# Kernel optimization log

Hardware: AMD Instinct MI355X
Metric: run time of the kernel (lower is better)

## Reference

```python
import jax, jax.numpy as jnp
import numpy as np

K_NEIGHBORS = 9
BN_EPS = 1e-5


def _bn(x, g, b, m, v):
    # inference-mode BatchNorm over channel (last) axis
    return (x - m) * (g / jnp.sqrt(v + BN_EPS)) + b


def _sincos_1d(dim, pos):
    half = dim // 2
    omega = 1.0 / (10000.0 ** (jnp.arange(half, dtype=jnp.float32) / half))
    ang = pos[:, None] * omega[None, :]
    return jnp.concatenate([jnp.sin(ang), jnp.cos(ang)], axis=1)


def _pos_embed_2d(dim, H, W):
    # standard 2D sin-cos positional embedding, (N, dim)
    yy, xx = jnp.meshgrid(jnp.arange(H, dtype=jnp.float32), jnp.arange(W, dtype=jnp.float32), indexing='ij')
    emb_h = _sincos_1d(dim // 2, yy.reshape(-1))
    emb_w = _sincos_1d(dim // 2, xx.reshape(-1))
    return jnp.concatenate([emb_h, emb_w], axis=1)


def setup_inputs() -> dict:
    key = jax.random.key(0)
    ks = jax.random.split(key, 8)
    B, C, H, W = 8, 192, 56, 56
    C2 = 2 * C
    Cg = C2 // 4  # per-group channels for grouped 1x1 conv
    x = jax.random.normal(ks[0], (B, C, H, W), jnp.float32)
    inp = {
        'x': x,
        'fc1_w': jax.random.normal(ks[1], (C, C), jnp.float32) * 0.05,
        'fc1_b': jnp.zeros((C,), jnp.float32),
        'bn1_g': jnp.ones((C,), jnp.float32),
        'bn1_b': jnp.zeros((C,), jnp.float32),
        'bn1_m': jax.random.normal(ks[2], (C,), jnp.float32) * 0.1,
        'bn1_v': jax.random.uniform(ks[3], (C,), jnp.float32, 0.5, 1.5),
        'gc_w': jax.random.normal(ks[4], (4, Cg, Cg), jnp.float32) * 0.05,  # groups=4, (g, out_pg, in_pg)
        'gc_b': jnp.zeros((C2,), jnp.float32),
        'bng_g': jnp.ones((C2,), jnp.float32),
        'bng_b': jnp.zeros((C2,), jnp.float32),
        'bng_m': jax.random.normal(ks[5], (C2,), jnp.float32) * 0.1,
        'bng_v': jax.random.uniform(ks[6], (C2,), jnp.float32, 0.5, 1.5),
        'fc2_w': jax.random.normal(ks[7], (C, C2), jnp.float32) * 0.05,
        'fc2_b': jnp.zeros((C,), jnp.float32),
        'bn2_g': jnp.ones((C,), jnp.float32),
        'bn2_b': jnp.zeros((C,), jnp.float32),
        'bn2_m': jnp.zeros((C,), jnp.float32),
        'bn2_v': jnp.ones((C,), jnp.float32),
    }
    return inp


def reference(x, fc1_w, fc1_b, bn1_g, bn1_b, bn1_m, bn1_v,
              gc_w, gc_b, bng_g, bng_b, bng_m, bng_v,
              fc2_w, fc2_b, bn2_g, bn2_b, bn2_m, bn2_v):
    B, C, H, W = x.shape
    N = H * W
    shortcut = x
    # fc1: 1x1 conv + BN, working in (B, N, C) layout
    h = x.reshape(B, C, N).transpose(0, 2, 1)
    h = jnp.einsum('bnc,dc->bnd', h, fc1_w) + fc1_b
    h = _bn(h, bn1_g, bn1_b, bn1_m, bn1_v)
    # relative position bias (ViG-style: -2*pe@pe.T/dim)
    pe = _pos_embed_2d(C, H, W)                      # (N, C)
    rel = (-2.0 / C) * (pe @ pe.T)                   # (N, N)
    # dense dilated kNN graph on L2-normalized features
    xn = h / jnp.maximum(jnp.linalg.norm(h, axis=-1, keepdims=True), 1e-12)
    sq = jnp.sum(xn * xn, axis=-1, keepdims=True)    # (B, N, 1)
    dist = sq - 2.0 * jnp.einsum('bnc,bmc->bnm', xn, xn) + sq.transpose(0, 2, 1)
    dist = dist + rel[None]                          # (B, N, N)
    _, nn_idx = jax.lax.top_k(-dist, K_NEIGHBORS)    # (B, N, K), dilation=1
    # MRConv2d: max-relative aggregation
    x_j = h[jnp.arange(B)[:, None, None], nn_idx]    # (B, N, K, C) gather
    d = jnp.max(x_j - h[:, :, None, :], axis=2)      # (B, N, C)
    g = jnp.concatenate([h, d], axis=-1)             # (B, N, 2C)
    # grouped 1x1 conv (groups=4) + BN + GELU
    C2 = 2 * C
    Cg = C2 // 4
    gg = g.reshape(B, N, 4, Cg)
    y = jnp.einsum('bngc,gdc->bngd', gg, gc_w).reshape(B, N, C2) + gc_b
    y = jax.nn.gelu(_bn(y, bng_g, bng_b, bng_m, bng_v), approximate=False)
    # fc2: 1x1 conv + BN, residual
    o = jnp.einsum('bnc,dc->bnd', y, fc2_w) + fc2_b
    o = _bn(o, bn2_g, bn2_b, bn2_m, bn2_v)
    out = o.transpose(0, 2, 1).reshape(B, C, H, W) + shortcut
    return out
```

## Files before the change

### kernel.cpp

```cpp
#include <hip/hip_runtime.h>
#include <math.h>

#define BATCH 8
#define CH    192
#define WW    56
#define NPTS  3136
#define C2    384
#define CG    96
#define MT    32
#define MSPLIT 4
#define LK    12
#define NCAND (MSPLIT*LK)
#define NREF  16
#define MQ    (NPTS/MSPLIT)

typedef float f32x4 __attribute__((ext_vector_type(4)));
typedef short bf16x8 __attribute__((ext_vector_type(8)));

__device__ __forceinline__ float gelu_exact(float v) {
  return 0.5f * v * (1.0f + erff(v * 0.7071067811865475f));
}
__device__ __forceinline__ unsigned short f2bf(float f) {
  unsigned int u = __float_as_uint(f);
  u = u + 0x7fffu + ((u >> 16) & 1u);
  return (unsigned short)(u >> 16);
}
__device__ __forceinline__ float bf2f(unsigned short h) {
  return __uint_as_float(((unsigned int)h) << 16);
}
__device__ __forceinline__ void gl_lds16(const void* g, void* lds) {
  __builtin_amdgcn_global_load_lds(
      (const __attribute__((address_space(1))) unsigned int*)g,
      (__attribute__((address_space(3))) unsigned int*)lds, 16, 0, 0);
}
__device__ __forceinline__ unsigned fmono(float f) {
  unsigned u = __float_as_uint(f);
  return u ^ ((unsigned)((int)u >> 31) | 0x80000000u);
}
__device__ __forceinline__ unsigned umin32(unsigned a, unsigned b) { return a < b ? a : b; }
__device__ __forceinline__ unsigned umax32(unsigned a, unsigned b) { return a < b ? b : a; }

__global__ void prep_kernel(
    const float* __restrict__ fc1_w, const float* __restrict__ fc1_b,
    const float* __restrict__ bn1_g, const float* __restrict__ bn1_b,
    const float* __restrict__ bn1_m, const float* __restrict__ bn1_v,
    const float* __restrict__ gc_w,  const float* __restrict__ gc_b,
    const float* __restrict__ bng_g, const float* __restrict__ bng_b,
    const float* __restrict__ bng_m, const float* __restrict__ bng_v,
    const float* __restrict__ fc2_w, const float* __restrict__ fc2_b,
    const float* __restrict__ bn2_g, const float* __restrict__ bn2_b,
    const float* __restrict__ bn2_m, const float* __restrict__ bn2_v,
    float* __restrict__ w1, float* __restrict__ b1,
    unsigned short* __restrict__ wgh, unsigned short* __restrict__ wgl,
    float* __restrict__ bg,
    unsigned short* __restrict__ w2h, unsigned short* __restrict__ w2l,
    float* __restrict__ b2, float* __restrict__ ftab)
{
  int i = blockIdx.x * 256 + threadIdx.x;
  if (i < 36864) {
    int d = i / CH;
    float s = bn1_g[d] / sqrtf(bn1_v[d] + 1e-5f);
    w1[i] = fc1_w[i] * s;
  } else if (i < 37056) {
    int d = i - 36864;
    float s = bn1_g[d] / sqrtf(bn1_v[d] + 1e-5f);
    b1[d] = (fc1_b[d] - bn1_m[d]) * s + bn1_b[d];
  } else if (i < 73920) {
    int j = i - 37056;
    int o = j / CG;
    float s = bng_g[o] / sqrtf(bng_v[o] + 1e-5f);
    float v = gc_w[j] * s;
    unsigned short hi = f2bf(v);
    wgh[j] = hi;
    wgl[j] = f2bf(v - bf2f(hi));
  } else if (i < 74304) {
    int o = i - 73920;
    float s = bng_g[o] / sqrtf(bng_v[o] + 1e-5f);
    bg[o] = (gc_b[o] - bng_m[o]) * s + bng_b[o];
  } else if (i < 148032) {
    int j = i - 74304;
    int d = j / C2;
    float s = bn2_g[d] / sqrtf(bn2_v[d] + 1e-5f);
    float v = fc2_w[j] * s;
    unsigned short hi = f2bf(v);
    w2h[j] = hi;
    w2l[j] = f2bf(v - bf2f(hi));
  } else if (i < 148224) {
    int d = i - 148032;
    float s = bn2_g[d] / sqrtf(bn2_v[d] + 1e-5f);
    b2[d] = (fc2_b[d] - bn2_m[d]) * s + bn2_b[d];
  } else if (i < 148280) {
    int delta = i - 148224;
    float s = 0.f;
    for (int t = 0; t < 48; ++t) {
      float omega = powf(10000.f, -(float)t / 48.f);
      s += cosf((float)delta * omega);
    }
    ftab[delta] = s * (-2.0f / (float)CH);
  }
}

__global__ __launch_bounds__(256) void xt_kernel(
    const float* __restrict__ x, float* __restrict__ xt)
{
  __shared__ float T[64 * 65];
  const int tid = threadIdx.x;
  const int nt = blockIdx.x, kt = blockIdx.y, b = blockIdx.z;
  const int n0 = nt * 64, k0 = kt * 64;
  const float* xb = x + (size_t)b * CH * NPTS;
#pragma unroll
  for (int p = 0; p < 16; ++p) {
    int e = p * 256 + tid;
    int kk = e >> 6, r = e & 63;
    T[kk * 65 + r] = xb[(size_t)(k0 + kk) * NPTS + n0 + r];
  }
  __syncthreads();
#pragma unroll
  for (int p = 0; p < 4; ++p) {
    int e = p * 256 + tid;
    int r = e >> 4, k4 = (e & 15) << 2;
    float4 v;
    v.x = T[(k4 + 0) * 65 + r];
    v.y = T[(k4 + 1) * 65 + r];
    v.z = T[(k4 + 2) * 65 + r];
    v.w = T[(k4 + 3) * 65 + r];
    *(float4*)&xt[((size_t)b * NPTS + n0 + r) * CH + k0 + k4] = v;
  }
}

__global__ __launch_bounds__(256) void fc1_kernel(
    const float* __restrict__ xt, const float* __restrict__ w1,
    const float* __restrict__ b1, float* __restrict__ h)
{
  __shared__ float As[64*68];
  __shared__ float Bs[64*68];
  const int tid = threadIdx.x;
  const int ntile = blockIdx.x, dt = blockIdx.y, b = blockIdx.z;
  const int n0 = ntile * 64, d0 = dt * 64;
  const int ty = tid >> 4, tx = tid & 15;
  const float* xa = xt + ((size_t)b * NPTS + n0) * CH;
  const float* wb = w1 + (size_t)d0 * CH;
  const int tya = ty & 7, txa = tx & 7;
  float acc[4][4] = {};
  for (int k0 = 0; k0 < CH; k0 += 64) {
    if (k0) __syncthreads();
#pragma unroll
    for (int p = 0; p < 4; ++p) {
      int e = p * 256 + tid;
      int r = e >> 4, c4 = e & 15;
      int col = (c4 ^ ((r >> 2) & 7)) << 2;
      *(float4*)&As[r*68 + col] = *(const float4*)&xa[(size_t)r * CH + k0 + (c4 << 2)];
      *(float4*)&Bs[r*68 + col] = *(const float4*)&wb[(size_t)r * CH + k0 + (c4 << 2)];
    }
    __syncthreads();
#pragma unroll
    for (int kq = 0; kq < 16; ++kq) {
      const int ca = (kq ^ tya) << 2;
      const int cb = (kq ^ txa) << 2;
      float4 av[4], bv[4];
#pragma unroll
      for (int i = 0; i < 4; ++i) av[i] = *(const float4*)&As[(ty*4+i)*68 + ca];
#pragma unroll
      for (int j = 0; j < 4; ++j) bv[j] = *(const float4*)&Bs[(tx*4+j)*68 + cb];
#pragma unroll
      for (int i = 0; i < 4; ++i)
#pragma unroll
        for (int j = 0; j < 4; ++j)
          acc[i][j] += av[i].x*bv[j].x + av[i].y*bv[j].y + av[i].z*bv[j].z + av[i].w*bv[j].w;
    }
  }
#pragma unroll
  for (int i = 0; i < 4; ++i) {
    int n = n0 + ty*4 + i;
    float4 v;
    v.x = acc[i][0] + b1[d0 + tx*4 + 0];
    v.y = acc[i][1] + b1[d0 + tx*4 + 1];
    v.z = acc[i][2] + b1[d0 + tx*4 + 2];
    v.w = acc[i][3] + b1[d0 + tx*4 + 3];
    *(float4*)&h[((size_t)b * NPTS + n) * CH + d0 + tx*4] = v;
  }
}

__global__ __launch_bounds__(256) void norm_kernel(
    const float* __restrict__ h, float* __restrict__ xnf,
    unsigned short* __restrict__ xhi, unsigned short* __restrict__ xlo,
    float* __restrict__ sqv)
{
  const int lane = threadIdx.x & 63;
  const int row = blockIdx.x * 4 + (threadIdx.x >> 6);
  const float* hr = h + (size_t)row * CH;
  float v0 = hr[lane], v1 = hr[lane + 64], v2 = hr[lane + 128];
  float s = v0*v0 + v1*v1 + v2*v2;
#pragma unroll
  for (int o = 32; o > 0; o >>= 1) s += __shfl_xor(s, o);
  float inv = 1.0f / fmaxf(sqrtf(s), 1e-12f);
  float x0 = v0 * inv, x1 = v1 * inv, x2 = v2 * inv;
  size_t base = (size_t)row * CH;
  xnf[base + lane      ] = x0;
  xnf[base + lane + 64 ] = x1;
  xnf[base + lane + 128] = x2;
  unsigned short h0 = f2bf(x0), h1 = f2bf(x1), h2 = f2bf(x2);
  xhi[base + lane      ] = h0;
  xhi[base + lane + 64 ] = h1;
  xhi[base + lane + 128] = h2;
  xlo[base + lane      ] = f2bf(x0 - bf2f(h0));
  xlo[base + lane + 64 ] = f2bf(x1 - bf2f(h1));
  xlo[base + lane + 128] = f2bf(x2 - bf2f(h2));
  if (lane == 0) sqv[row] = s * inv * inv;
}

__global__ __launch_bounds__(256, 3) void topk_kernel(
    const unsigned short* __restrict__ xhi, const unsigned short* __restrict__ xlo,
    const float* __restrict__ fts_g,
    unsigned* __restrict__ pd)
{
  __shared__ __align__(16) char LDSbuf[2 * 24576];
  __shared__ float ft[64];

  const int tid  = threadIdx.x;
  const int lane = tid & 63;
  const int w    = tid >> 6;
  const int bid  = blockIdx.x;
  const int b    = bid & 7;
  const int r_   = bid >> 3;
  const int ms   = r_ / 49;
  const int nt   = r_ % 49;
  const int n0 = nt * 64;
  const size_t rowbase = (size_t)b * NPTS;

  if (tid < 64) ft[tid] = (tid < 56) ? fts_g[tid] : 0.0f;

  const int ar = lane & 15;
  const int hi = lane >> 4;
  const int ak = hi * 8;

  const int n_b = n0 + w * 16 + ar;
  bf16x8 bhi[6], blo[6];
  {
    const unsigned short* pbh = xhi + (rowbase + n_b) * CH + ak;
    const unsigned short* pbl = xlo + (rowbase + n_b) * CH + ak;
#pragma unroll
    for (int c = 0; c < 6; ++c) {
      bhi[c] = *(const bf16x8*)(pbh + c * 32);
      blo[c] = *(const bf16x8*)(pbl + c * 32);
    }
  }
  const int yn_l = n_b / WW, xn_l = n_b % WW;

  unsigned ld[LK];
#pragma unroll
  for (int k = 0; k < LK; ++k) ld[k] = 0xFFFFFFFFu;

  int srcb[6];
#pragma unroll
  for (int j = 0; j < 6; ++j) {
    int L = (w & 1) * 6144 + j * 1024 + lane * 16;
    int r = L / 384, off = L % 384;
    srcb[j] = r * 384 + (off ^ ((r & 7) << 4));
  }
  const int ldsb = (w >= 2 ? 12288 : 0) + (w & 1) * 6144;

  const int mbase = ms * MQ;
  const char* gb = (w < 2 ? (const char*)xhi : (const char*)xlo)
                   + (rowbase + mbase) * (CH * 2);

#define STAGE(BUF) do {                                                     \
  _Pragma("unroll")                                                         \
  for (int j = 0; j < 6; ++j)                                               \
    gl_lds16(gb + srcb[j], LDSbuf + (BUF) * 24576 + ldsb + j * 1024);       \
} while (0)

  STAGE(0);
  gb += 12288;

  int ym0 = ms * 14, xm0 = 0;

  for (int tt = 0; tt < 25; ++tt) {
    __syncthreads();
    if (tt + 1 < 25) { STAGE((tt + 1) & 1); gb += 12288; }

    const int bufb = (tt & 1) * 24576;
    const int swz = (ar & 7) << 4;
    const float fdy0 = ft[abs(yn_l - ym0)];
    const float fdy1 = ft[abs(yn_l - ym0 - 1)];
    const int nrt = (tt == 24) ? 1 : 2;
#pragma unroll
    for (int rt = 0; rt < 2; ++rt) {
      if (rt >= nrt) break;
      const int rA = rt * 16 + ar;
      f32x4 a_hh = {}, a_hl = {}, a_lh = {};
#pragma unroll
      for (int c = 0; c < 6; ++c) {
        int off = bufb + rA * 384 + ((c * 64 + hi * 16) ^ swz);
        bf16x8 ah = *(const bf16x8*)(LDSbuf + off);
        bf16x8 al = *(const bf16x8*)(LDSbuf + off + 12288);
        a_hh = __builtin_amdgcn_mfma_f32_16x16x32_bf16(ah, bhi[c], a_hh, 0, 0, 0);
        a_hl = __builtin_amdgcn_mfma_f32_16x16x32_bf16(ah, blo[c], a_hl, 0, 0, 0);
        a_lh = __builtin_amdgcn_mfma_f32_16x16x32_bf16(al, bhi[c], a_lh, 0, 0, 0);
      }
      f32x4 s4;
#pragma unroll
      for (int i = 0; i < 4; ++i) s4[i] = a_hh[i] + (a_hl[i] + a_lh[i]);

      const int locb = tt * MT + rt * 16 + hi * 4;
      unsigned kk[4];
#pragma unroll
      for (int i = 0; i < 4; ++i) {
        int xm = xm0 + rt * 16 + hi * 4 + i;
        const bool wrap = (xm >= WW);
        if (wrap) xm -= WW;
        int dx = xn_l - xm; dx = dx < 0 ? -dx : dx;
        float d_ = (wrap ? fdy1 : fdy0) + ft[dx] - 2.0f * s4[i];
        kk[i] = (fmono(d_) & 0xFFFFFC00u) | (unsigned)(locb + i);
      }
      {
        unsigned sa = umax32(kk[0], kk[1]), sb = umin32(kk[0], kk[1]);
        unsigned sc = umax32(kk[2], kk[3]), sd = umin32(kk[2], kk[3]);
        unsigned v0 = umax32(sa, sc), t1 = umin32(sa, sc);
        unsigned t2 = umax32(sb, sd), v3 = umin32(sb, sd);
        unsigned v1 = umax32(t1, t2), v2 = umin32(t1, t2);
        unsigned l4 = umin32(ld[4], v0), g4 = umax32(ld[4], v0);
        unsigned l5 = umin32(ld[5], v1), g5 = umax32(ld[5], v1);
        unsigned l6 = umin32(ld[6], v2), g6 = umax32(ld[6], v2);
        unsigned l7 = umin32(ld[7], v3), g7 = umax32(ld[7], v3);
        unsigned a0 = umin32(ld[0], l4), b0 = umax32(ld[0], l4);
        unsigned a1 = umin32(ld[1], l5), b1 = umax32(ld[1], l5);
        unsigned a2 = umin32(ld[2], l6), b2 = umax32(ld[2], l6);
        unsigned a3 = umin32(ld[3], l7), b3 = umax32(ld[3], l7);
        unsigned q0 = umin32(a0, a2), q2 = umax32(a0, a2);
        unsigned q1 = umin32(a1, a3), q3 = umax32(a1, a3);
        unsigned r0 = umin32(b0, b2), r2 = umax32(b0, b2);
        unsigned r1 = umin32(b1, b3), r3 = umax32(b1, b3);
        ld[0] = umin32(q0, q1); ld[1] = umax32(q0, q1);
        ld[2] = umin32(q2, q3); ld[3] = umax32(q2, q3);
        ld[4] = umin32(r0, r1); ld[5] = umax32(r0, r1);
        ld[6] = umin32(r2, r3); ld[7] = umax32(r2, r3);
        unsigned e0 = umin32(ld[8],  g4);
        unsigned e1 = umin32(ld[9],  g5);
        unsigned e2 = umin32(ld[10], g6);
        unsigned e3 = umin32(ld[11], g7);
        unsigned f0 = umin32(e0, e2), f2 = umax32(e0, e2);
        unsigned f1 = umin32(e1, e3), f3 = umax32(e1, e3);
        ld[8]  = umin32(f0, f1); ld[9]  = umax32(f0, f1);
        ld[10] = umin32(f2, f3); ld[11] = umax32(f2, f3);
      }
    }
    xm0 += MT;
    if (xm0 >= WW) { xm0 -= WW; ym0 += 1; }
  }

  __syncthreads();
  unsigned* Md = (unsigned*)LDSbuf;
#pragma unroll
  for (int k = 0; k < LK; ++k) Md[tid * LK + k] = ld[k];
  __syncthreads();
  if (tid < 64) {
    const int wv = tid >> 4, arr = tid & 15;
    const int n = n0 + tid;
    int lb[4];
#pragma unroll
    for (int hq = 0; hq < 4; ++hq) lb[hq] = (wv * 64 + hq * 16 + arr) * LK;
    int p0 = 0, p1 = 0, p2 = 0, p3 = 0;
    unsigned* od = pd + ((rowbase + n) * MSPLIT + ms) * LK;
    for (int k = 0; k < LK; ++k) {
      unsigned bk = Md[lb[0] + p0]; int bq = 0;
      unsigned v1 = Md[lb[1] + p1];
      if (v1 < bk) { bk = v1; bq = 1; }
      unsigned v2 = Md[lb[2] + p2];
      if (v2 < bk) { bk = v2; bq = 2; }
      unsigned v3 = Md[lb[3] + p3];
      if (v3 < bk) { bk = v3; bq = 3; }
      if (bq == 0) { if (p0 < LK-1) ++p0; else Md[lb[0]+p0] = 0xFFFFFFFFu; }
      else if (bq == 1) { if (p1 < LK-1) ++p1; else Md[lb[1]+p1] = 0xFFFFFFFFu; }
      else if (bq == 2) { if (p2 < LK-1) ++p2; else Md[lb[2]+p2] = 0xFFFFFFFFu; }
      else              { if (p3 < LK-1) ++p3; else Md[lb[3]+p3] = 0xFFFFFFFFu; }
      od[k] = bk;
    }
  }
#undef STAGE
}

__global__ __launch_bounds__(256) void refine_kernel(
    const unsigned* __restrict__ pd,
    const float* __restrict__ xn, const float* __restrict__ sqv,
    const float* __restrict__ fts_g, int* __restrict__ nn)
{
  __shared__ unsigned allk[4][NCAND];
  __shared__ int      ci_s[4][NREF];
  __shared__ float ft[56];
  const int tid = threadIdx.x;
  const int w = tid >> 6, lane = tid & 63;
  if (tid < 56) ft[tid] = fts_g[tid];
  const int row = blockIdx.x * 4 + w;
  const int b = row / NPTS;
  const int n_loc = row - b * NPTS;

  if (lane < NCAND) allk[w][lane] = pd[(size_t)row * NCAND + lane];
  __syncthreads();
  if (lane < NCAND) {
    unsigned k0 = allk[w][lane];
    int rank = 0;
    for (int j = 0; j < NCAND; ++j) {
      unsigned kj = allk[w][j];
      rank += (kj < k0 || (kj == k0 && j < lane)) ? 1 : 0;
    }
    if (rank < NREF) ci_s[w][rank] = (lane / LK) * MQ + (int)(k0 & 1023u);
  }
  __syncthreads();

  const float* xrow = xn + (size_t)row * CH;
  float a0 = xrow[lane], a1 = xrow[lane + 64], a2 = xrow[lane + 128];
  const int yn_ = n_loc / WW, xq_ = n_loc % WW;
  const size_t xbase = (size_t)b * NPTS * CH;

  int cm[NREF];
  float xv0[NREF], xv1[NREF], xv2[NREF];
#pragma unroll
  for (int c = 0; c < NREF; ++c) {
    int m = ci_s[w][c];
    cm[c] = m;
    const float* xm = xn + xbase + (size_t)m * CH;
    xv0[c] = xm[lane];
    xv1[c] = xm[lane + 64];
    xv2[c] = xm[lane + 128];
  }

  float myd = INFINITY; int myi = 0x7fffffff;
#pragma unroll
  for (int c = 0; c < NREF; ++c) {
    float s = a0 * xv0[c] + a1 * xv1[c] + a2 * xv2[c];
#pragma unroll
    for (int o = 32; o > 0; o >>= 1) s += __shfl_xor(s, o);
    if (lane == c) {
      int m = cm[c];
      int ym = m / WW, xm_ = m % WW;
      int dy = yn_ - ym; dy = dy < 0 ? -dy : dy;
      int dx = xq_ - xm_; dx = dx < 0 ? -dx : dx;
      myd = sqv[(size_t)b * NPTS + m] - 2.0f * s + (ft[dy] + ft[dx]);
      myi = m;
    }
  }
  if (lane < NREF) {
    int rank = 0;
    for (int j = 0; j < NREF; ++j) {
      float dj = __shfl(myd, j); int ij = __shfl(myi, j);
      rank += (dj < myd || (dj == myd && ij < myi)) ? 1 : 0;
    }
    if (rank < 9) nn[(size_t)row * 9 + rank] = myi;
  }
}

__global__ __launch_bounds__(256, 4) void gc_kernel(
    const float* __restrict__ h, const int* __restrict__ nn,
    const unsigned short* __restrict__ wgh, const unsigned short* __restrict__ wgl,
    const float* __restrict__ bg, unsigned short* __restrict__ y)
{
  __shared__ __align__(16) char Wb[2 * 18432];
  __shared__ int nns[576];
  const int tid = threadIdx.x;
  const int lane = tid & 63;
  const int w = tid >> 6;
  const int rt = blockIdx.x, g = blockIdx.y;
  const int n0g = rt * 64;
  const int b = n0g / NPTS;
  const size_t rowbase = (size_t)b * NPTS;
  const int cb = (g & 1) * CG;
  const int cn = lane & 15;
  const int kq = lane >> 4;
  const bool isD = (g >= 2);

  {
    const char* gh = (const char*)wgh + (size_t)g * 96 * 192;
    const char* gl = (const char*)wgl + (size_t)g * 96 * 192;
    for (int c = tid; c < 1152; c += 256) {
      int L = c * 16;
      int row = L / 192;
      int slot = (L % 192) >> 4;
      int sb = row * 192 + ((slot ^ (row & 3)) << 4);
      gl_lds16(gh + sb, Wb + L);
      gl_lds16(gl + sb, Wb + 18432 + L);
    }
  }
  if (isD) {
    for (int e = tid; e < 576; e += 256)
      nns[e] = nn[(size_t)(n0g + e / 9) * 9 + (e % 9)];
  }
  __syncthreads();

  const int rloc = w * 16 + cn;
  const int nb = n0g + rloc;
  bf16x8 gh8[3], gl8[3];
#pragma unroll
  for (int c = 0; c < 3; ++c) {
    const float* base = h + (size_t)nb * CH + cb + c * 32 + kq * 8;
    float4 x0 = *(const float4*)base;
    float4 x1 = *(const float4*)(base + 4);
    if (isD) {
      float4 m0 = make_float4(-INFINITY, -INFINITY, -INFINITY, -INFINITY);
      float4 m1 = m0;
#pragma unroll
      for (int k = 0; k < 9; ++k) {
        const float* nbase = h + (rowbase + nns[rloc * 9 + k]) * CH + cb + c * 32 + kq * 8;
        float4 n0v = *(const float4*)nbase;
        float4 n1v = *(const float4*)(nbase + 4);
        m0.x = fmaxf(m0.x, n0v.x); m0.y = fmaxf(m0.y, n0v.y);
        m0.z = fmaxf(m0.z, n0v.z); m0.w = fmaxf(m0.w, n0v.w);
        m1.x = fmaxf(m1.x, n1v.x); m1.y = fmaxf(m1.y, n1v.y);
        m1.z = fmaxf(m1.z, n1v.z); m1.w = fmaxf(m1.w, n1v.w);
      }
      x0.x = m0.x - x0.x; x0.y = m0.y - x0.y; x0.z = m0.z - x0.z; x0.w = m0.w - x0.w;
      x1.x = m1.x - x1.x; x1.y = m1.y - x1.y; x1.z = m1.z - x1.z; x1.w = m1.w - x1.w;
    }
    float v[8];
    *(float4*)&v[0] = x0;
    *(float4*)&v[4] = x1;
#pragma unroll
    for (int j = 0; j < 8; ++j) {
      unsigned short hh = f2bf(v[j]);
      gh8[c][j] = (short)hh;
      gl8[c][j] = (short)f2bf(v[j] - bf2f(hh));
    }
  }

#pragma unroll
  for (int sub = 0; sub < 6; ++sub) {
    f32x4 acc = {};
#pragma unroll
    for (int c = 0; c < 3; ++c) {
      int row = sub * 16 + cn;
      int slot = c * 4 + kq;
      int off = row * 192 + ((slot ^ (row & 3)) << 4);
      bf16x8 ah = *(const bf16x8*)(Wb + off);
      bf16x8 al = *(const bf16x8*)(Wb + 18432 + off);
      acc = __builtin_amdgcn_mfma_f32_16x16x32_bf16(ah, gh8[c], acc, 0, 0, 0);
      acc = __builtin_amdgcn_mfma_f32_16x16x32_bf16(ah, gl8[c], acc, 0, 0, 0);
      acc = __builtin_amdgcn_mfma_f32_16x16x32_bf16(al, gh8[c], acc, 0, 0, 0);
    }
    const int ocb = g * CG + sub * 16 + kq * 4;
    unsigned short pk[4];
#pragma unroll
    for (int i = 0; i < 4; ++i)
      pk[i] = f2bf(gelu_exact(acc[i] + bg[ocb + i]));
    *(ushort4*)&y[(size_t)nb * C2 + ocb] = *(ushort4*)pk;
  }
}

__global__ __launch_bounds__(256, 4) void fc2_kernel(
    const unsigned short* __restrict__ yv,
    const unsigned short* __restrict__ w2h, const unsigned short* __restrict__ w2l,
    const float* __restrict__ b2, const float* __restrict__ x, float* __restrict__ out)
{
  __shared__ __align__(16) char Wb[2 * 12288];
  const int tid = threadIdx.x;
  const int lane = tid & 63;
  const int w = tid >> 6;
  const int rt = blockIdx.x, dg = blockIdx.y;
  const int n0g = rt * 64;
  const int b = n0g / NPTS;
  const int nloc0 = n0g - b * NPTS;
  const int cn = lane & 15;
  const int kk0 = (lane >> 4) * 8;

  bf16x8 yb[12];
  {
    const unsigned short* yp = yv + (size_t)(n0g + w * 16 + cn) * C2 + kk0;
#pragma unroll
    for (int c = 0; c < 12; ++c) yb[c] = *(const bf16x8*)(yp + c * 32);
  }

  int srcb[3], dstb[3];
#pragma unroll
  for (int j = 0; j < 3; ++j) {
    int L = (w * 3 + j) * 1024 + lane * 16;
    int r = L / 768, off = L % 768;
    srcb[j] = r * 768 + (off ^ ((r & 7) << 4));
    dstb[j] = (w * 3 + j) * 1024;
  }

  const char* gh = (const char*)w2h + (size_t)dg * 64 * 768;
  const char* gl = (const char*)w2l + (size_t)dg * 64 * 768;
  const int rr = cn;
  const int swz = (rr & 7) << 4;
  const int nsp = nloc0 + w * 16 + cn;

  for (int ds = 0; ds < 4; ++ds) {
    __syncthreads();
#pragma unroll
    for (int j = 0; j < 3; ++j) {
      gl_lds16(gh + ds * 12288 + srcb[j], Wb + dstb[j]);
      gl_lds16(gl + ds * 12288 + srcb[j], Wb + 12288 + dstb[j]);
    }
    __syncthreads();

    f32x4 acc_h = {}, acc_l = {};
#pragma unroll
    for (int c = 0; c < 12; ++c) {
      int off = rr * 768 + ((c * 64 + (lane >> 4) * 16) ^ swz);
      bf16x8 ah = *(const bf16x8*)(Wb + off);
      bf16x8 al = *(const bf16x8*)(Wb + 12288 + off);
      acc_h = __builtin_amdgcn_mfma_f32_16x16x32_bf16(ah, yb[c], acc_h, 0, 0, 0);
      acc_l = __builtin_amdgcn_mfma_f32_16x16x32_bf16(al, yb[c], acc_l, 0, 0, 0);
    }
    const int d0 = dg * 64 + ds * 16;
#pragma unroll
    for (int i = 0; i < 4; ++i) {
      int d = d0 + (lane >> 4) * 4 + i;
      size_t gi = ((size_t)b * CH + d) * NPTS + nsp;
      out[gi] = acc_h[i] + acc_l[i] + b2[d] + x[gi];
    }
  }
}

extern "C" void kernel_launch(void* const* d_in, const int* in_sizes, int n_in,
                              void* d_out, int out_size, void* d_ws, size_t ws_size,
                              hipStream_t stream) {
  const float* x     = (const float*)d_in[0];
  const float* fc1_w = (const float*)d_in[1];
  const float* fc1_b = (const float*)d_in[2];
  const float* bn1_g = (const float*)d_in[3];
  const float* bn1_b = (const float*)d_in[4];
  const float* bn1_m = (const float*)d_in[5];
  const float* bn1_v = (const float*)d_in[6];
  const float* gc_w  = (const float*)d_in[7];
  const float* gc_b  = (const float*)d_in[8];
  const float* bng_g = (const float*)d_in[9];
  const float* bng_b = (const float*)d_in[10];
  const float* bng_m = (const float*)d_in[11];
  const float* bng_v = (const float*)d_in[12];
  const float* fc2_w = (const float*)d_in[13];
  const float* fc2_b = (const float*)d_in[14];
  const float* bn2_g = (const float*)d_in[15];
  const float* bn2_b = (const float*)d_in[16];
  const float* bn2_m = (const float*)d_in[17];
  const float* bn2_v = (const float*)d_in[18];

  float* ws = (float*)d_ws;
  size_t o = 0;
  float* W1 = ws + o; o += 36864;
  float* B1 = ws + o; o += 192;
  unsigned short* WGH = (unsigned short*)(ws + o); o += 18432;
  unsigned short* WGL = (unsigned short*)(ws + o); o += 18432;
  float* BG = ws + o; o += 384;
  unsigned short* W2H = (unsigned short*)(ws + o); o += 36864;
  unsigned short* W2L = (unsigned short*)(ws + o); o += 36864;
  float* B2 = ws + o; o += 192;
  float* FT = ws + o; o += 64;
  float* H  = ws + o; o += (size_t)25088 * 192;
  float* SQ = ws + o; o += 25088;
  int*   NN = (int*)(ws + o); o += 25088 * 9;
  float* SCR = ws + o;
  float* XT  = SCR;
  unsigned short* XHI = (unsigned short*)SCR;
  unsigned short* XLO = XHI + (size_t)4816896;
  float* XN  = SCR + (size_t)4816896;
  unsigned short* YB = (unsigned short*)XN;
  unsigned* PD = (unsigned*)(XN + (size_t)4816896);
  (void)ws_size; (void)in_sizes; (void)n_in; (void)out_size;

  hipLaunchKernelGGL(prep_kernel, dim3(580), dim3(256), 0, stream,
                     fc1_w, fc1_b, bn1_g, bn1_b, bn1_m, bn1_v,
                     gc_w, gc_b, bng_g, bng_b, bng_m, bng_v,
                     fc2_w, fc2_b, bn2_g, bn2_b, bn2_m, bn2_v,
                     W1, B1, WGH, WGL, BG, W2H, W2L, B2, FT);
  hipLaunchKernelGGL(xt_kernel, dim3(49, 3, 8), dim3(256), 0, stream, x, XT);
  hipLaunchKernelGGL(fc1_kernel, dim3(49, 3, 8), dim3(256), 0, stream, XT, W1, B1, H);
  hipLaunchKernelGGL(norm_kernel, dim3(6272), dim3(256), 0, stream, H, XN, XHI, XLO, SQ);
  hipLaunchKernelGGL(topk_kernel, dim3(49 * MSPLIT * 8), dim3(256), 0, stream, XHI, XLO, FT, PD);
  hipLaunchKernelGGL(refine_kernel, dim3(6272), dim3(256), 0, stream, PD, XN, SQ, FT, NN);
  hipLaunchKernelGGL(gc_kernel, dim3(392, 4), dim3(256), 0, stream, H, NN, WGH, WGL, BG, YB);
  hipLaunchKernelGGL(fc2_kernel, dim3(392, 3), dim3(256), 0, stream, YB, W2H, W2L, B2, x, (float*)d_out);
}
```

Baseline: 361.1 us.

## Double query tile per topk block to reuse staged candidate tiles

```diff
diff --git a/kernel.cpp b/kernel.cpp
--- a/kernel.cpp
+++ b/kernel.cpp
@@ -13,6 +13,7 @@
 #define NCAND (MSPLIT*LK)
 #define NREF  16
 #define MQ    (NPTS/MSPLIT)
+#define NT128 25
 
 typedef float f32x4 __attribute__((ext_vector_type(4)));
 typedef short bf16x8 __attribute__((ext_vector_type(8)));
@@ -39,6 +40,38 @@
 }
 __device__ __forceinline__ unsigned umin32(unsigned a, unsigned b) { return a < b ? a : b; }
 __device__ __forceinline__ unsigned umax32(unsigned a, unsigned b) { return a < b ? b : a; }
+
+__device__ __forceinline__ void merge12(unsigned (&ld)[LK], const unsigned* kk) {
+  unsigned sa = umax32(kk[0], kk[1]), sb = umin32(kk[0], kk[1]);
+  unsigned sc = umax32(kk[2], kk[3]), sd = umin32(kk[2], kk[3]);
+  unsigned v0 = umax32(sa, sc), t1 = umin32(sa, sc);
+  unsigned t2 = umax32(sb, sd), v3 = umin32(sb, sd);
+  unsigned v1 = umax32(t1, t2), v2 = umin32(t1, t2);
+  unsigned l4 = umin32(ld[4], v0), g4 = umax32(ld[4], v0);
+  unsigned l5 = umin32(ld[5], v1), g5 = umax32(ld[5], v1);
+  unsigned l6 = umin32(ld[6], v2), g6 = umax32(ld[6], v2);
+  unsigned l7 = umin32(ld[7], v3), g7 = umax32(ld[7], v3);
+  unsigned a0 = umin32(ld[0], l4), b0 = umax32(ld[0], l4);
+  unsigned a1 = umin32(ld[1], l5), b1 = umax32(ld[1], l5);
+  unsigned a2 = umin32(ld[2], l6), b2 = umax32(ld[2], l6);
+  unsigned a3 = umin32(ld[3], l7), b3 = umax32(ld[3], l7);
+  unsigned q0 = umin32(a0, a2), q2 = umax32(a0, a2);
+  unsigned q1 = umin32(a1, a3), q3 = umax32(a1, a3);
+  unsigned r0 = umin32(b0, b2), r2 = umax32(b0, b2);
+  unsigned r1 = umin32(b1, b3), r3 = umax32(b1, b3);
+  ld[0] = umin32(q0, q1); ld[1] = umax32(q0, q1);
+  ld[2] = umin32(q2, q3); ld[3] = umax32(q2, q3);
+  ld[4] = umin32(r0, r1); ld[5] = umax32(r0, r1);
+  ld[6] = umin32(r2, r3); ld[7] = umax32(r2, r3);
+  unsigned e0 = umin32(ld[8],  g4);
+  unsigned e1 = umin32(ld[9],  g5);
+  unsigned e2 = umin32(ld[10], g6);
+  unsigned e3 = umin32(ld[11], g7);
+  unsigned f0 = umin32(e0, e2), f2 = umax32(e0, e2);
+  unsigned f1 = umin32(e1, e3), f3 = umax32(e1, e3);
+  ld[8]  = umin32(f0, f1); ld[9]  = umax32(f0, f1);
+  ld[10] = umin32(f2, f3); ld[11] = umax32(f2, f3);
+}
 
 __global__ void prep_kernel(
     const float* __restrict__ fc1_w, const float* __restrict__ fc1_b,
@@ -209,7 +242,7 @@
   if (lane == 0) sqv[row] = s * inv * inv;
 }
 
-__global__ __launch_bounds__(256, 3) void topk_kernel(
+__global__ __launch_bounds__(256, 2) void topk_kernel(
     const unsigned short* __restrict__ xhi, const unsigned short* __restrict__ xlo,
     const float* __restrict__ fts_g,
     unsigned* __restrict__ pd)
@@ -223,9 +256,9 @@
   const int bid  = blockIdx.x;
   const int b    = bid & 7;
   const int r_   = bid >> 3;
-  const int ms   = r_ / 49;
-  const int nt   = r_ % 49;
-  const int n0 = nt * 64;
+  const int ms   = r_ / NT128;
+  const int nt   = r_ % NT128;
+  const int n0 = nt * 128;
   const size_t rowbase = (size_t)b * NPTS;
 
   if (tid < 64) ft[tid] = (tid < 56) ? fts_g[tid] : 0.0f;
@@ -234,22 +267,28 @@
   const int hi = lane >> 4;
   const int ak = hi * 8;
 
-  const int n_b = n0 + w * 16 + ar;
-  bf16x8 bhi[6], blo[6];
+  int nb0 = n0 + w * 16 + ar;       if (nb0 > NPTS - 1) nb0 = NPTS - 1;
+  int nb1 = n0 + 64 + w * 16 + ar;  if (nb1 > NPTS - 1) nb1 = NPTS - 1;
+  bf16x8 b0h[6], b0l[6], b1h[6], b1l[6];
   {
-    const unsigned short* pbh = xhi + (rowbase + n_b) * CH + ak;
-    const unsigned short* pbl = xlo + (rowbase + n_b) * CH + ak;
+    const unsigned short* p0h = xhi + (rowbase + nb0) * CH + ak;
+    const unsigned short* p0l = xlo + (rowbase + nb0) * CH + ak;
+    const unsigned short* p1h = xhi + (rowbase + nb1) * CH + ak;
+    const unsigned short* p1l = xlo + (rowbase + nb1) * CH + ak;
 #pragma unroll
     for (int c = 0; c < 6; ++c) {
-      bhi[c] = *(const bf16x8*)(pbh + c * 32);
-      blo[c] = *(const bf16x8*)(pbl + c * 32);
-    }
-  }
-  const int yn_l = n_b / WW, xn_l = n_b % WW;
-
-  unsigned ld[LK];
-#pragma unroll
-  for (int k = 0; k < LK; ++k) ld[k] = 0xFFFFFFFFu;
+      b0h[c] = *(const bf16x8*)(p0h + c * 32);
+      b0l[c] = *(const bf16x8*)(p0l + c * 32);
+      b1h[c] = *(const bf16x8*)(p1h + c * 32);
+      b1l[c] = *(const bf16x8*)(p1l + c * 32);
+    }
+  }
+  const int yn0 = nb0 / WW, xq0 = nb0 % WW;
+  const int yn1 = nb1 / WW, xq1 = nb1 % WW;
+
+  unsigned ld0[LK], ld1[LK];
+#pragma unroll
+  for (int k = 0; k < LK; ++k) { ld0[k] = 0xFFFFFFFFu; ld1[k] = 0xFFFFFFFFu; }
 
   int srcb[6];
 #pragma unroll
@@ -281,26 +320,35 @@
 
     const int bufb = (tt & 1) * 24576;
     const int swz = (ar & 7) << 4;
-    const float fdy0 = ft[abs(yn_l - ym0)];
-    const float fdy1 = ft[abs(yn_l - ym0 - 1)];
+    const float fdy00 = ft[abs(yn0 - ym0)];
+    const float fdy01 = ft[abs(yn0 - ym0 - 1)];
+    const float fdy10 = ft[abs(yn1 - ym0)];
+    const float fdy11 = ft[abs(yn1 - ym0 - 1)];
     const int nrt = (tt == 24) ? 1 : 2;
 #pragma unroll
     for (int rt = 0; rt < 2; ++rt) {
       if (rt >= nrt) break;
       const int rA = rt * 16 + ar;
-      f32x4 a_hh = {}, a_hl = {}, a_lh = {};
+      f32x4 a0hh = {}, a0hl = {}, a0lh = {};
+      f32x4 a1hh = {}, a1hl = {}, a1lh = {};
 #pragma unroll
       for (int c = 0; c < 6; ++c) {
         int off = bufb + rA * 384 + ((c * 64 + hi * 16) ^ swz);
         bf16x8 ah = *(const bf16x8*)(LDSbuf + off);
         bf16x8 al = *(const bf16x8*)(LDSbuf + off + 12288);
-        a_hh = __builtin_amdgcn_mfma_f32_16x16x32_bf16(ah, bhi[c], a_hh, 0, 0, 0);
-        a_hl = __builtin_amdgcn_mfma_f32_16x16x32_bf16(ah, blo[c], a_hl, 0, 0, 0);
-        a_lh = __builtin_amdgcn_mfma_f32_16x16x32_bf16(al, bhi[c], a_lh, 0, 0, 0);
+        a0hh = __builtin_amdgcn_mfma_f32_16x16x32_bf16(ah, b0h[c], a0hh, 0, 0, 0);
+        a0hl = __builtin_amdgcn_mfma_f32_16x16x32_bf16(ah, b0l[c], a0hl, 0, 0, 0);
+        a0lh = __builtin_amdgcn_mfma_f32_16x16x32_bf16(al, b0h[c], a0lh, 0, 0, 0);
+        a1hh = __builtin_amdgcn_mfma_f32_16x16x32_bf16(ah, b1h[c], a1hh, 0, 0, 0);
+        a1hl = __builtin_amdgcn_mfma_f32_16x16x32_bf16(ah, b1l[c], a1hl, 0, 0, 0);
+        a1lh = __builtin_amdgcn_mfma_f32_16x16x32_bf16(al, b1h[c], a1lh, 0, 0, 0);
       }
-      f32x4 s4;
-#pragma unroll
-      for (int i = 0; i < 4; ++i) s4[i] = a_hh[i] + (a_hl[i] + a_lh[i]);
+      f32x4 s40, s41;
+#pragma unroll
+      for (int i = 0; i < 4; ++i) {
+        s40[i] = a0hh[i] + (a0hl[i] + a0lh[i]);
+        s41[i] = a1hh[i] + (a1hl[i] + a1lh[i]);
+      }
 
       const int locb = tt * MT + rt * 16 + hi * 4;
       unsigned kk[4];
@@ -309,41 +357,21 @@
         int xm = xm0 + rt * 16 + hi * 4 + i;
         const bool wrap = (xm >= WW);
         if (wrap) xm -= WW;
-        int dx = xn_l - xm; dx = dx < 0 ? -dx : dx;
-        float d_ = (wrap ? fdy1 : fdy0) + ft[dx] - 2.0f * s4[i];
+        int dx = xq0 - xm; dx = dx < 0 ? -dx : dx;
+        float d_ = (wrap ? fdy01 : fdy00) + ft[dx] - 2.0f * s40[i];
         kk[i] = (fmono(d_) & 0xFFFFFC00u) | (unsigned)(locb + i);
       }
-      {
-        unsigned sa = umax32(kk[0], kk[1]), sb = umin32(kk[0], kk[1]);
-        unsigned sc = umax32(kk[2], kk[3]), sd = umin32(kk[2], kk[3]);
-        unsigned v0 = umax32(sa, sc), t1 = umin32(sa, sc);
-        unsigned t2 = umax32(sb, sd), v3 = umin32(sb, sd);
-        unsigned v1 = umax32(t1, t2), v2 = umin32(t1, t2);
-        unsigned l4 = umin32(ld[4], v0), g4 = umax32(ld[4], v0);
-        unsigned l5 = umin32(ld[5], v1), g5 = umax32(ld[5], v1);
-        unsigned l6 = umin32(ld[6], v2), g6 = umax32(ld[6], v2);
-        unsigned l7 = umin32(ld[7], v3), g7 = umax32(ld[7], v3);
-        unsigned a0 = umin32(ld[0], l4), b0 = umax32(ld[0], l4);
-        unsigned a1 = umin32(ld[1], l5), b1 = umax32(ld[1], l5);
-        unsigned a2 = umin32(ld[2], l6), b2 = umax32(ld[2], l6);
-        unsigned a3 = umin32(ld[3], l7), b3 = umax32(ld[3], l7);
-        unsigned q0 = umin32(a0, a2), q2 = umax32(a0, a2);
-        unsigned q1 = umin32(a1, a3), q3 = umax32(a1, a3);
-        unsigned r0 = umin32(b0, b2), r2 = umax32(b0, b2);
-        unsigned r1 = umin32(b1, b3), r3 = umax32(b1, b3);
-        ld[0] = umin32(q0, q1); ld[1] = umax32(q0, q1);
-        ld[2] = umin32(q2, q3); ld[3] = umax32(q2, q3);
-        ld[4] = umin32(r0, r1); ld[5] = umax32(r0, r1);
-        ld[6] = umin32(r2, r3); ld[7] = umax32(r2, r3);
-        unsigned e0 = umin32(ld[8],  g4);
-        unsigned e1 = umin32(ld[9],  g5);
-        unsigned e2 = umin32(ld[10], g6);
-        unsigned e3 = umin32(ld[11], g7);
-        unsigned f0 = umin32(e0, e2), f2 = umax32(e0, e2);
-        unsigned f1 = umin32(e1, e3), f3 = umax32(e1, e3);
-        ld[8]  = umin32(f0, f1); ld[9]  = umax32(f0, f1);
-        ld[10] = umin32(f2, f3); ld[11] = umax32(f2, f3);
+      merge12(ld0, kk);
+#pragma unroll
+      for (int i = 0; i < 4; ++i) {
+        int xm = xm0 + rt * 16 + hi * 4 + i;
+        const bool wrap = (xm >= WW);
+        if (wrap) xm -= WW;
+        int dx = xq1 - xm; dx = dx < 0 ? -dx : dx;
+        float d_ = (wrap ? fdy11 : fdy10) + ft[dx] - 2.0f * s41[i];
+        kk[i] = (fmono(d_) & 0xFFFFFC00u) | (unsigned)(locb + i);
       }
+      merge12(ld1, kk);
     }
     xm0 += MT;
     if (xm0 >= WW) { xm0 -= WW; ym0 += 1; }
@@ -352,29 +380,35 @@
   __syncthreads();
   unsigned* Md = (unsigned*)LDSbuf;
 #pragma unroll
-  for (int k = 0; k < LK; ++k) Md[tid * LK + k] = ld[k];
+  for (int k = 0; k < LK; ++k) {
+    Md[tid * 24 + k] = ld0[k];
+    Md[tid * 24 + 12 + k] = ld1[k];
+  }
   __syncthreads();
-  if (tid < 64) {
-    const int wv = tid >> 4, arr = tid & 15;
-    const int n = n0 + tid;
-    int lb[4];
-#pragma unroll
-    for (int hq = 0; hq < 4; ++hq) lb[hq] = (wv * 64 + hq * 16 + arr) * LK;
-    int p0 = 0, p1 = 0, p2 = 0, p3 = 0;
-    unsigned* od = pd + ((rowbase + n) * MSPLIT + ms) * LK;
-    for (int k = 0; k < LK; ++k) {
-      unsigned bk = Md[lb[0] + p0]; int bq = 0;
-      unsigned v1 = Md[lb[1] + p1];
-      if (v1 < bk) { bk = v1; bq = 1; }
-      unsigned v2 = Md[lb[2] + p2];
-      if (v2 < bk) { bk = v2; bq = 2; }
-      unsigned v3 = Md[lb[3] + p3];
-      if (v3 < bk) { bk = v3; bq = 3; }
-      if (bq == 0) { if (p0 < LK-1) ++p0; else Md[lb[0]+p0] = 0xFFFFFFFFu; }
-      else if (bq == 1) { if (p1 < LK-1) ++p1; else Md[lb[1]+p1] = 0xFFFFFFFFu; }
-      else if (bq == 2) { if (p2 < LK-1) ++p2; else Md[lb[2]+p2] = 0xFFFFFFFFu; }
-      else              { if (p3 < LK-1) ++p3; else Md[lb[3]+p3] = 0xFFFFFFFFu; }
-      od[k] = bk;
+  if (tid < 128) {
+    const int set = tid >> 6, t6 = tid & 63;
+    const int wv = t6 >> 4, arr = t6 & 15;
+    const int n = n0 + set * 64 + wv * 16 + arr;
+    if (n < NPTS) {
+      int lb[4];
+#pragma unroll
+      for (int hq = 0; hq < 4; ++hq) lb[hq] = (wv * 64 + hq * 16 + arr) * 24 + set * 12;
+      int p0 = 0, p1 = 0, p2 = 0, p3 = 0;
+      unsigned* od = pd + ((rowbase + n) * MSPLIT + ms) * LK;
+      for (int k = 0; k < LK; ++k) {
+        unsigned bk = Md[lb[0] + p0]; int bq = 0;
+        unsigned v1 = Md[lb[1] + p1];
+        if (v1 < bk) { bk = v1; bq = 1; }
+        unsigned v2 = Md[lb[2] + p2];
+        if (v2 < bk) { bk = v2; bq = 2; }
+        unsigned v3 = Md[lb[3] + p3];
+        if (v3 < bk) { bk = v3; bq = 3; }
+        if (bq == 0) { if (p0 < LK-1) ++p0; else Md[lb[0]+p0] = 0xFFFFFFFFu; }
+        else if (bq == 1) { if (p1 < LK-1) ++p1; else Md[lb[1]+p1] = 0xFFFFFFFFu; }
+        else if (bq == 2) { if (p2 < LK-1) ++p2; else Md[lb[2]+p2] = 0xFFFFFFFFu; }
+        else              { if (p3 < LK-1) ++p3; else Md[lb[3]+p3] = 0xFFFFFFFFu; }
+        od[k] = bk;
+      }
     }
   }
 #undef STAGE
@@ -665,7 +699,7 @@
   hipLaunchKernelGGL(xt_kernel, dim3(49, 3, 8), dim3(256), 0, stream, x, XT);
   hipLaunchKernelGGL(fc1_kernel, dim3(49, 3, 8), dim3(256), 0, stream, XT, W1, B1, H);
   hipLaunchKernelGGL(norm_kernel, dim3(6272), dim3(256), 0, stream, H, XN, XHI, XLO, SQ);
-  hipLaunchKernelGGL(topk_kernel, dim3(49 * MSPLIT * 8), dim3(256), 0, stream, XHI, XLO, FT, PD);
+  hipLaunchKernelGGL(topk_kernel, dim3(NT128 * MSPLIT * 8), dim3(256), 0, stream, XHI, XLO, FT, PD);
   hipLaunchKernelGGL(refine_kernel, dim3(6272), dim3(256), 0, stream, PD, XN, SQ, FT, NN);
   hipLaunchKernelGGL(gc_kernel, dim3(392, 4), dim3(256), 0, stream, H, NN, WGH, WGL, BG, YB);
   hipLaunchKernelGGL(fc2_kernel, dim3(392, 3), dim3(256), 0, stream, YB, W2H, W2L, B2, x, (float*)d_out);
```

New measurement: 374.8 us. +3.8%, slower.
